# Kernel tuning notes

Measured on AMD Instinct MI355X. Metric: run time of the kernel, lower is better.

Reference implementation:

```python
import jax, jax.numpy as jnp
import numpy as np

N, C, D = 131072, 1024, 64

def setup_inputs() -> dict:
    key = jax.random.key(0)
    k1, k2, k3 = jax.random.split(key, 3)
    inputs = jax.random.normal(k1, (N, D), dtype=jnp.float32)
    centers = jax.random.normal(k2, (C, D), dtype=jnp.float32)
    coefs = jax.random.uniform(k3, (C,), dtype=jnp.float32) / C
    max_avg_distance = jnp.ones((1,), dtype=jnp.float32)
    return {"inputs": inputs, "centers": centers, "coefs": coefs,
            "max_avg_distance": max_avg_distance}

def _pairwise_l2(x, c):
    x2 = jnp.sum(x * x, axis=-1, keepdims=True)          # (N, 1)
    c2 = jnp.sum(c * c, axis=-1)                          # (C,)
    d2 = x2 + c2 - 2.0 * jnp.einsum('nd,cd->nc', x, c)    # (N, C)
    return jnp.sqrt(jnp.maximum(d2, 0.0))

def reference(inputs, centers, coefs, max_avg_distance):
    x = inputs.reshape(inputs.shape[0], -1)               # flatten(inputs, 1)
    distances = _pairwise_l2(x, centers)                  # (N, C)
    c = jnp.abs(coefs)
    s = jnp.sum(c)
    c = jnp.where(s == 0.0, c, c / s)                     # normalize unless sum==0
    weighted_avg = distances @ c                          # (N,)
    return max_avg_distance - weighted_avg                # broadcast (1,)-(N,) -> (N,)
```

## Files before the change

kernel.cpp:

```cpp
#include <hip/hip_runtime.h>
#include <hip/hip_bf16.h>
#include <cstdint>

#define DIM 64
#define NC  1024
#define PF  2

typedef __attribute__((ext_vector_type(8))) __bf16 bf16x8;
typedef __attribute__((ext_vector_type(8))) short short8;
typedef __attribute__((ext_vector_type(4))) float f32x4;
typedef __attribute__((ext_vector_type(4))) unsigned int uint4v;

static __device__ __forceinline__ unsigned short f32_to_bf16_rne(float f) {
    unsigned int u = __builtin_bit_cast(unsigned int, f);
    unsigned int r = u + 0x7FFFu + ((u >> 16) & 1u);
    return (unsigned short)(r >> 16);
}
static __device__ __forceinline__ float bf16_bits_to_f32(unsigned short h) {
    return __builtin_bit_cast(float, (unsigned int)h << 16);
}

__global__ void coef_kernel(const float* __restrict__ coefs,
                            float2* __restrict__ wc2) {
    __shared__ float red[NC];
    const int c = threadIdx.x;
    const float a = fabsf(coefs[c]);
    red[c] = a;
    __syncthreads();
    for (int s = NC / 2; s > 0; s >>= 1) {
        if (c < s) red[c] += red[c + s];
        __syncthreads();
    }
    const float sum = red[0];
    const float w = (sum == 0.0f) ? a : a / sum;
    wc2[c].x = w;
}

__global__ void center_kernel(const float* __restrict__ centers,
                              float2* __restrict__ wc2,
                              short8* __restrict__ bfrag) {
    const int c = blockIdx.x * 64 + threadIdx.x;
    const float4* row = (const float4*)(centers + (size_t)c * DIM);

    float vals[DIM];
    float c2 = 0.0f;
#pragma unroll
    for (int q = 0; q < DIM / 4; ++q) {
        float4 v = row[q];
        vals[q * 4 + 0] = v.x; vals[q * 4 + 1] = v.y;
        vals[q * 4 + 2] = v.z; vals[q * 4 + 3] = v.w;
        c2 = fmaf(v.x, v.x, c2); c2 = fmaf(v.y, v.y, c2);
        c2 = fmaf(v.z, v.z, c2); c2 = fmaf(v.w, v.w, c2);
    }
    const unsigned short hi = f32_to_bf16_rne(c2);
    const unsigned short lo = f32_to_bf16_rne(c2 - bf16_bits_to_f32(hi));
    const unsigned int packed = (unsigned int)hi | ((unsigned int)lo << 16);
    wc2[c].y = __builtin_bit_cast(float, packed);

    const int tile = c >> 4;
    const int colL = c & 15;
#pragma unroll
    for (int kb = 0; kb < 2; ++kb) {
#pragma unroll
        for (int h = 0; h < 4; ++h) {
            short8 p;
#pragma unroll
            for (int j = 0; j < 8; ++j) {
                float v = -2.0f * vals[kb * 32 + h * 8 + j];
                p[j] = (short)f32_to_bf16_rne(v);
            }
            bfrag[(tile * 2 + kb) * 64 + (h * 16 + colL)] = p;
        }
    }
}

__global__ __launch_bounds__(256, 4) void dist_kernel(
    const float* __restrict__ x,
    const float2* __restrict__ wc2,
    const bf16x8* __restrict__ bfrag,
    const float* __restrict__ madp,
    float* __restrict__ out)
{
    const int lane = threadIdx.x & 63;
    const int wave = threadIdx.x >> 6;
    const int lo = lane & 15;
    const int hi = lane >> 4;
    const int rg    = wave >> 1;
    const int halfC = wave & 1;
    const int R = blockIdx.x * 64;

    __shared__ short8 alds[8][64];
    __shared__ __align__(16) float x2lds[64];
    __shared__ float part[4][32];

    {
        const int row = R + wave * 16 + lo;
        const float* rp = x + (size_t)row * DIM + hi * 8;
        float s2 = 0.0f;
#pragma unroll
        for (int kb = 0; kb < 2; ++kb) {
            float4 v0 = *(const float4*)(rp + kb * 32);
            float4 v1 = *(const float4*)(rp + kb * 32 + 4);
            float vv[8] = {v0.x, v0.y, v0.z, v0.w, v1.x, v1.y, v1.z, v1.w};
            short8 p;
#pragma unroll
            for (int j = 0; j < 8; ++j) {
                s2 = fmaf(vv[j], vv[j], s2);
                p[j] = (short)f32_to_bf16_rne(vv[j]);
            }
            alds[wave * 2 + kb][lane] = p;
        }
        s2 += __shfl_xor(s2, 16, 64);
        s2 += __shfl_xor(s2, 32, 64);
        if (hi == 0) x2lds[wave * 16 + lo] = s2;
    }
    __syncthreads();

    bf16x8 afrag[2][2];
    f32x4 x2c[2];
#pragma unroll
    for (int g = 0; g < 2; ++g) {
        const int t16 = rg * 2 + g;
#pragma unroll
        for (int kb = 0; kb < 2; ++kb)
            afrag[g][kb] = __builtin_bit_cast(bf16x8, alds[t16 * 2 + kb][lane]);
        x2c[g] = *(const f32x4*)&x2lds[t16 * 16 + hi * 4];
    }

    const unsigned int ao = (hi == 0) ? 0x3F803F80u : 0u;
    const bf16x8 afones = __builtin_bit_cast(bf16x8, (uint4v){ao, 0u, 0u, 0u});

    float sum[2][4];
#pragma unroll
    for (int g = 0; g < 2; ++g)
#pragma unroll
        for (int b = 0; b < 4; ++b) sum[g][b] = 0.0f;

    const int tbase = halfC * 32;
    const bf16x8* bp = bfrag + lane;
    const float2* wp = wc2 + lo;

    bf16x8 pb0[PF], pb1[PF];
    float2 pwc[PF];
#pragma unroll
    for (int j = 0; j < PF; ++j) {
        const int t = tbase + j;
        pb0[j] = bp[t * 128];
        pb1[j] = bp[t * 128 + 64];
        pwc[j] = wp[t * 16];
    }

#pragma unroll 1
    for (int i = 0; i < 32; i += PF) {
#pragma unroll
        for (int j = 0; j < PF; ++j) {
            const float2 wc = pwc[j];
            const float w = wc.x;
            const unsigned int packed = __builtin_bit_cast(unsigned int, wc.y);
            const bf16x8 bc2 = __builtin_bit_cast(bf16x8,
                (uint4v){(hi == 0) ? packed : 0u, 0u, 0u, 0u});
            const bf16x8 b0 = pb0[j];
            const bf16x8 b1 = pb1[j];

            {
                const int nxt = i + j + PF;
                const int tn = tbase + ((nxt < 32) ? nxt : 0);
                pb0[j] = bp[tn * 128];
                pb1[j] = bp[tn * 128 + 64];
                pwc[j] = wp[tn * 16];
            }

#pragma unroll
            for (int g = 0; g < 2; ++g) {
                f32x4 acc;
                acc = __builtin_amdgcn_mfma_f32_16x16x32_bf16(afones, bc2, x2c[g], 0, 0, 0);
                acc = __builtin_amdgcn_mfma_f32_16x16x32_bf16(afrag[g][0], b0, acc, 0, 0, 0);
                acc = __builtin_amdgcn_mfma_f32_16x16x32_bf16(afrag[g][1], b1, acc, 0, 0, 0);
#pragma unroll
                for (int b = 0; b < 4; ++b) {
                    float d = __builtin_amdgcn_sqrtf(fabsf(acc[b]));
                    sum[g][b] = fmaf(w, d, sum[g][b]);
                }
            }
        }
    }

#pragma unroll
    for (int g = 0; g < 2; ++g) {
#pragma unroll
        for (int b = 0; b < 4; ++b) {
            float v = sum[g][b];
            v += __shfl_xor(v, 1, 64);
            v += __shfl_xor(v, 2, 64);
            v += __shfl_xor(v, 4, 64);
            v += __shfl_xor(v, 8, 64);
            if (lo == 0) part[wave][g * 16 + hi * 4 + b] = v;
        }
    }
    __syncthreads();

    const int tid = threadIdx.x;
    if (tid < 64) {
        const int r2 = tid >> 5;
        const int r  = tid & 31;
        const float s = part[r2 * 2][r] + part[r2 * 2 + 1][r];
        out[R + r2 * 32 + r] = madp[0] - s;
    }
}

extern "C" void kernel_launch(void* const* d_in, const int* in_sizes, int n_in,
                              void* d_out, int out_size, void* d_ws, size_t ws_size,
                              hipStream_t stream) {
    const float* x       = (const float*)d_in[0];
    const float* centers = (const float*)d_in[1];
    const float* coefs   = (const float*)d_in[2];
    const float* mad     = (const float*)d_in[3];
    float* out = (float*)d_out;

    float2* wc2   = (float2*)d_ws;
    short8* bfrag = (short8*)((char*)d_ws + NC * sizeof(float2));

    const int N = in_sizes[0] / DIM;

    coef_kernel<<<1, NC, 0, stream>>>(coefs, wc2);
    center_kernel<<<NC / 64, 64, 0, stream>>>(centers, wc2, bfrag);
    dist_kernel<<<N / 64, 256, 0, stream>>>(x, wc2, (const bf16x8*)bfrag, mad, out);
}
```

Before: 46.10 us.

## Switch distance GEMM to 32x32x16 bf16 MFMA with per-wave register A fragments

Replaces the 16x16x32 MFMA tiling with 32x32x16 MFMA. Each wave now covers 32 rows by 512 centers, loads its A fragments straight into registers instead of staging them through LDS, and drops the first __syncthreads. The center fragment layout is rearranged to match. The larger MFMA shape raises math per operand load and removes the LDS round-trip. In exchange it needs more accumulator registers and more B loads per tile, and each wave now converts 32 rows of x, so neighbouring waves duplicate the x load and bf16 conversion.

Result: slower. 50.51 us (+9.6%).

```diff
diff --git a/kernel.cpp b/kernel.cpp
--- a/kernel.cpp
+++ b/kernel.cpp
@@ -6,10 +6,10 @@
 #define NC  1024
 #define PF  2
 
-typedef __attribute__((ext_vector_type(8))) __bf16 bf16x8;
-typedef __attribute__((ext_vector_type(8))) short short8;
-typedef __attribute__((ext_vector_type(4))) float f32x4;
-typedef __attribute__((ext_vector_type(4))) unsigned int uint4v;
+typedef __attribute__((ext_vector_type(8)))  __bf16 bf16x8;
+typedef __attribute__((ext_vector_type(8)))  short  short8;
+typedef __attribute__((ext_vector_type(16))) float  f32x16;
+typedef __attribute__((ext_vector_type(4)))  unsigned int uint4v;
 
 static __device__ __forceinline__ unsigned short f32_to_bf16_rne(float f) {
     unsigned int u = __builtin_bit_cast(unsigned int, f);
@@ -57,19 +57,19 @@
     const unsigned int packed = (unsigned int)hi | ((unsigned int)lo << 16);
     wc2[c].y = __builtin_bit_cast(float, packed);
 
-    const int tile = c >> 4;
-    const int colL = c & 15;
-#pragma unroll
-    for (int kb = 0; kb < 2; ++kb) {
-#pragma unroll
-        for (int h = 0; h < 4; ++h) {
+    const int tile = c >> 5;
+    const int col  = c & 31;
+#pragma unroll
+    for (int ks = 0; ks < 4; ++ks) {
+#pragma unroll
+        for (int h = 0; h < 2; ++h) {
             short8 p;
 #pragma unroll
             for (int j = 0; j < 8; ++j) {
-                float v = -2.0f * vals[kb * 32 + h * 8 + j];
+                float v = -2.0f * vals[ks * 16 + h * 8 + j];
                 p[j] = (short)f32_to_bf16_rne(v);
             }
-            bfrag[(tile * 2 + kb) * 64 + (h * 16 + colL)] = p;
+            bfrag[(tile * 4 + ks) * 64 + (h * 32 + col)] = p;
         }
     }
 }
@@ -83,24 +83,24 @@
 {
     const int lane = threadIdx.x & 63;
     const int wave = threadIdx.x >> 6;
-    const int lo = lane & 15;
-    const int hi = lane >> 4;
-    const int rg    = wave >> 1;
-    const int halfC = wave & 1;
+    const int col  = lane & 31;
+    const int kh   = lane >> 5;
+    const int rg   = wave >> 1;
+    const int half = wave & 1;
     const int R = blockIdx.x * 64;
 
-    __shared__ short8 alds[8][64];
-    __shared__ __align__(16) float x2lds[64];
+    __shared__ float x2lds[4][32];
     __shared__ float part[4][32];
 
+    bf16x8 afrag[4];
+    float s2 = 0.0f;
     {
-        const int row = R + wave * 16 + lo;
-        const float* rp = x + (size_t)row * DIM + hi * 8;
-        float s2 = 0.0f;
-#pragma unroll
-        for (int kb = 0; kb < 2; ++kb) {
-            float4 v0 = *(const float4*)(rp + kb * 32);
-            float4 v1 = *(const float4*)(rp + kb * 32 + 4);
+        const int row = R + rg * 32 + col;
+        const float* rp = x + (size_t)row * DIM + kh * 8;
+#pragma unroll
+        for (int ks = 0; ks < 4; ++ks) {
+            float4 v0 = *(const float4*)(rp + ks * 16);
+            float4 v1 = *(const float4*)(rp + ks * 16 + 4);
             float vv[8] = {v0.x, v0.y, v0.z, v0.w, v1.x, v1.y, v1.z, v1.w};
             short8 p;
 #pragma unroll
@@ -108,94 +108,81 @@
                 s2 = fmaf(vv[j], vv[j], s2);
                 p[j] = (short)f32_to_bf16_rne(vv[j]);
             }
-            alds[wave * 2 + kb][lane] = p;
+            afrag[ks] = __builtin_bit_cast(bf16x8, p);
         }
-        s2 += __shfl_xor(s2, 16, 64);
         s2 += __shfl_xor(s2, 32, 64);
-        if (hi == 0) x2lds[wave * 16 + lo] = s2;
-    }
-    __syncthreads();
-
-    bf16x8 afrag[2][2];
-    f32x4 x2c[2];
-#pragma unroll
-    for (int g = 0; g < 2; ++g) {
-        const int t16 = rg * 2 + g;
-#pragma unroll
-        for (int kb = 0; kb < 2; ++kb)
-            afrag[g][kb] = __builtin_bit_cast(bf16x8, alds[t16 * 2 + kb][lane]);
-        x2c[g] = *(const f32x4*)&x2lds[t16 * 16 + hi * 4];
-    }
-
-    const unsigned int ao = (hi == 0) ? 0x3F803F80u : 0u;
+        if (kh == 0) x2lds[wave][col] = s2;
+    }
+    f32x16 x2init;
+#pragma unroll
+    for (int reg = 0; reg < 16; ++reg)
+        x2init[reg] = x2lds[wave][(reg & 3) + 8 * (reg >> 2) + 4 * kh];
+
+    const unsigned int ao = (kh == 0) ? 0x3F803F80u : 0u;
     const bf16x8 afones = __builtin_bit_cast(bf16x8, (uint4v){ao, 0u, 0u, 0u});
 
-    float sum[2][4];
-#pragma unroll
-    for (int g = 0; g < 2; ++g)
-#pragma unroll
-        for (int b = 0; b < 4; ++b) sum[g][b] = 0.0f;
-
-    const int tbase = halfC * 32;
+    float sum[16];
+#pragma unroll
+    for (int r = 0; r < 16; ++r) sum[r] = 0.0f;
+
+    const int tbase = half * 16;
     const bf16x8* bp = bfrag + lane;
-    const float2* wp = wc2 + lo;
-
-    bf16x8 pb0[PF], pb1[PF];
+    const float2* wp = wc2 + col;
+
+    bf16x8 pb[PF][4];
     float2 pwc[PF];
 #pragma unroll
     for (int j = 0; j < PF; ++j) {
         const int t = tbase + j;
-        pb0[j] = bp[t * 128];
-        pb1[j] = bp[t * 128 + 64];
-        pwc[j] = wp[t * 16];
+#pragma unroll
+        for (int ks = 0; ks < 4; ++ks) pb[j][ks] = bp[(t * 4 + ks) * 64];
+        pwc[j] = wp[t * 32];
     }
 
 #pragma unroll 1
-    for (int i = 0; i < 32; i += PF) {
+    for (int i = 0; i < 16; i += PF) {
 #pragma unroll
         for (int j = 0; j < PF; ++j) {
             const float2 wc = pwc[j];
             const float w = wc.x;
             const unsigned int packed = __builtin_bit_cast(unsigned int, wc.y);
             const bf16x8 bc2 = __builtin_bit_cast(bf16x8,
-                (uint4v){(hi == 0) ? packed : 0u, 0u, 0u, 0u});
-            const bf16x8 b0 = pb0[j];
-            const bf16x8 b1 = pb1[j];
+                (uint4v){(kh == 0) ? packed : 0u, 0u, 0u, 0u});
+            bf16x8 b0 = pb[j][0], b1 = pb[j][1], b2 = pb[j][2], b3 = pb[j][3];
 
             {
                 const int nxt = i + j + PF;
-                const int tn = tbase + ((nxt < 32) ? nxt : 0);
-                pb0[j] = bp[tn * 128];
-                pb1[j] = bp[tn * 128 + 64];
-                pwc[j] = wp[tn * 16];
-            }
-
-#pragma unroll
-            for (int g = 0; g < 2; ++g) {
-                f32x4 acc;
-                acc = __builtin_amdgcn_mfma_f32_16x16x32_bf16(afones, bc2, x2c[g], 0, 0, 0);
-                acc = __builtin_amdgcn_mfma_f32_16x16x32_bf16(afrag[g][0], b0, acc, 0, 0, 0);
-                acc = __builtin_amdgcn_mfma_f32_16x16x32_bf16(afrag[g][1], b1, acc, 0, 0, 0);
-#pragma unroll
-                for (int b = 0; b < 4; ++b) {
-                    float d = __builtin_amdgcn_sqrtf(fabsf(acc[b]));
-                    sum[g][b] = fmaf(w, d, sum[g][b]);
-                }
+                const int tn = tbase + ((nxt < 16) ? nxt : 0);
+#pragma unroll
+                for (int ks = 0; ks < 4; ++ks) pb[j][ks] = bp[(tn * 4 + ks) * 64];
+                pwc[j] = wp[tn * 32];
+            }
+
+            f32x16 acc;
+            acc = __builtin_amdgcn_mfma_f32_32x32x16_bf16(afones, bc2, x2init, 0, 0, 0);
+            acc = __builtin_amdgcn_mfma_f32_32x32x16_bf16(afrag[0], b0, acc, 0, 0, 0);
+            acc = __builtin_amdgcn_mfma_f32_32x32x16_bf16(afrag[1], b1, acc, 0, 0, 0);
+            acc = __builtin_amdgcn_mfma_f32_32x32x16_bf16(afrag[2], b2, acc, 0, 0, 0);
+            acc = __builtin_amdgcn_mfma_f32_32x32x16_bf16(afrag[3], b3, acc, 0, 0, 0);
+
+#pragma unroll
+            for (int r = 0; r < 16; ++r) {
+                float d = __builtin_amdgcn_sqrtf(fabsf(acc[r]));
+                sum[r] = fmaf(w, d, sum[r]);
             }
         }
     }
 
 #pragma unroll
-    for (int g = 0; g < 2; ++g) {
-#pragma unroll
-        for (int b = 0; b < 4; ++b) {
-            float v = sum[g][b];
-            v += __shfl_xor(v, 1, 64);
-            v += __shfl_xor(v, 2, 64);
-            v += __shfl_xor(v, 4, 64);
-            v += __shfl_xor(v, 8, 64);
-            if (lo == 0) part[wave][g * 16 + hi * 4 + b] = v;
-        }
+    for (int reg = 0; reg < 16; ++reg) {
+        float v = sum[reg];
+        v += __shfl_xor(v, 1, 64);
+        v += __shfl_xor(v, 2, 64);
+        v += __shfl_xor(v, 4, 64);
+        v += __shfl_xor(v, 8, 64);
+        v += __shfl_xor(v, 16, 64);
+        if (col == 0)
+            part[wave][(reg & 3) + 8 * (reg >> 2) + 4 * kh] = v;
     }
     __syncthreads();
 
```
